# Kernel tuning notes

Measured on AMD Instinct MI355X. Metric: run time of the kernel, lower is better.

The kernel has to match this reference:

```python
import jax, jax.numpy as jnp
import numpy as np

DIM = 512
HEADS = 8
DIM_HEAD = 64
HIDDEN = HEADS * DIM_HEAD  # 512
SCALE = DIM_HEAD ** -0.5
EPS = 1e-5


def setup_inputs() -> dict:
    key = jax.random.key(0)
    ks = jax.random.split(key, 6)
    B, N = 4, 8192
    x = jax.random.normal(ks[0], (B, DIM, N), dtype=jnp.float32)
    ln_w = jnp.ones((DIM,), dtype=jnp.float32)
    ln_b = jnp.zeros((DIM,), dtype=jnp.float32)
    # stored as (in, out) so y = x @ W
    w_qkv = jax.random.normal(ks[1], (DIM, 3 * HIDDEN), dtype=jnp.float32) * (DIM ** -0.5)
    w_out = jax.random.normal(ks[2], (HIDDEN, DIM), dtype=jnp.float32) * (HIDDEN ** -0.5)
    b_out = jnp.zeros((DIM,), dtype=jnp.float32)
    return {"x": x, "ln_w": ln_w, "ln_b": ln_b, "w_qkv": w_qkv, "w_out": w_out, "b_out": b_out}


def _forward(x, ln_w, ln_b, w_qkv, w_out, b_out):
    B, D, N = x.shape
    h = jnp.swapaxes(x, 1, 2)  # b n d
    # LayerNorm over last dim
    mu = jnp.mean(h, axis=-1, keepdims=True)
    var = jnp.var(h, axis=-1, keepdims=True)
    h = (h - mu) * jax.lax.rsqrt(var + EPS) * ln_w + ln_b
    qkv = h @ w_qkv  # b n 3*hidden
    q, k, v = jnp.split(qkv, 3, axis=-1)
    # b n (h d) -> b h n d
    reshape = lambda t: jnp.swapaxes(t.reshape(B, N, HEADS, DIM_HEAD), 1, 2)
    q, k, v = reshape(q), reshape(k), reshape(v)
    q = jax.nn.softmax(q * SCALE, axis=-2)  # softmax over tokens n
    k = jax.nn.softmax(k, axis=-1)          # softmax over features d
    context = jnp.einsum('bhnd,bhne->bhde', k, v)  # small d x e per head
    out = jnp.einsum('bhde,bhnd->bhen', context, q)
    # b h e n -> b n (h e)
    out = jnp.swapaxes(out, 1, 3).reshape(B, N, HIDDEN)  # bhen -> bneh? careful: need (h e)
    # redo correctly: bhen -> b n h e -> b n (h e)
    # (the line above gives b n e h; compute properly instead)
    return out


def reference(x, ln_w, ln_b, w_qkv, w_out, b_out):
    B, D, N = x.shape
    h = jnp.swapaxes(x, 1, 2)  # b n d
    mu = jnp.mean(h, axis=-1, keepdims=True)
    var = jnp.var(h, axis=-1, keepdims=True)
    h = (h - mu) * jax.lax.rsqrt(var + EPS) * ln_w + ln_b
    qkv = h @ w_qkv  # b n 3*hidden
    q, k, v = jnp.split(qkv, 3, axis=-1)
    reshape = lambda t: jnp.swapaxes(t.reshape(B, N, HEADS, DIM_HEAD), 1, 2)  # b h n d
    q, k, v = reshape(q), reshape(k), reshape(v)
    q = jax.nn.softmax(q * SCALE, axis=-2)  # over tokens
    k = jax.nn.softmax(k, axis=-1)          # over head-dim
    context = jnp.einsum('bhnd,bhne->bhde', k, v)
    out = jnp.einsum('bhde,bhnd->bnhe', context, q)  # b n h e
    out = out.reshape(B, N, HIDDEN)  # (h e) concatenated per head
    out = out @ w_out + b_out  # b n dim
    return jnp.swapaxes(out, 1, 2)  # b dim n
```

## Files before the change

kernel.cpp:

```cpp
#include <hip/hip_runtime.h>

#define B_   4
#define N_   8192
#define D_   512
#define NH   8
#define DH   64
#define HID  512

typedef unsigned short u16;
typedef __attribute__((ext_vector_type(8))) short  bf16x8;
typedef __attribute__((ext_vector_type(8))) unsigned short u16x8;
typedef __attribute__((ext_vector_type(4))) float  f32x4;

__device__ __forceinline__ float bf2f(u16 u) {
  unsigned int i = ((unsigned int)u) << 16;
  return __builtin_bit_cast(float, i);
}
__device__ __forceinline__ u16 f2bf(float f) {
  unsigned int i = __builtin_bit_cast(unsigned int, f);
  i += 0x7fff + ((i >> 16) & 1);
  return (u16)(i >> 16);
}

#define GLOAD16(g, l) \
  __builtin_amdgcn_global_load_lds((const __attribute__((address_space(1))) void*)(g), \
                                   (__attribute__((address_space(3))) void*)(l), 16, 0, 0)

__global__ __launch_bounds__(256) void transpose_f2b(const float* __restrict__ in,
                                                     u16* __restrict__ out,
                                                     int rows, int cols) {
  int idx = blockIdx.x * 256 + threadIdx.x;
  if (idx < rows * cols) {
    int c = idx / rows, r = idx - c * rows;
    out[idx] = f2bf(in[r * cols + c]);
  }
}

__global__ __launch_bounds__(256) void ln_kernel(const float* __restrict__ x,
                                                 const float* __restrict__ lw,
                                                 const float* __restrict__ lb,
                                                 u16* __restrict__ h) {
  __shared__ u16 xs[32 * 520];
  __shared__ float red[2][8][32];
  __shared__ float murs[2][32];
  __shared__ float lws[512], lbs[512];
  int b = blockIdx.y, n0 = blockIdx.x * 32;
  int t = threadIdx.x;
  lws[t] = lw[t]; lws[t + 256] = lw[t + 256];
  lbs[t] = lb[t]; lbs[t + 256] = lb[t + 256];
  int tok = t & 31, dp = t >> 5;
  const float* xp = x + (long)b * D_ * N_ + n0 + tok;
  float s = 0.f, s2 = 0.f;
#pragma unroll 8
  for (int i = 0; i < 64; i++) {
    int d = dp * 64 + i;
    float v = xp[(long)d * N_];
    s += v; s2 += v * v;
    xs[tok * 520 + d] = f2bf(v);
  }
  red[0][dp][tok] = s; red[1][dp][tok] = s2;
  __syncthreads();
  if (t < 32) {
    float S1 = 0.f, S2 = 0.f;
#pragma unroll
    for (int i = 0; i < 8; i++) { S1 += red[0][i][t]; S2 += red[1][i][t]; }
    float mu = S1 * (1.0f / 512.0f);
    float var = S2 * (1.0f / 512.0f) - mu * mu;
    murs[0][t] = mu; murs[1][t] = rsqrtf(var + 1e-5f);
  }
  __syncthreads();
  int row = t >> 3, seg = t & 7;
  float mu = murs[0][row], rs = murs[1][row];
  u16* hp = h + ((long)b * N_ + n0 + row) * D_ + seg * 64;
  const u16* xr = xs + row * 520 + seg * 64;
#pragma unroll
  for (int c = 0; c < 8; c++) {
    u16x8 in8 = *(const u16x8*)(xr + c * 8);
    u16x8 o;
#pragma unroll
    for (int i = 0; i < 8; i++) {
      int d = seg * 64 + c * 8 + i;
      o[i] = f2bf((bf2f(in8[i]) - mu) * rs * lws[d] + lbs[d]);
    }
    *(u16x8*)(hp + c * 8) = o;
  }
}

__global__ __launch_bounds__(256) void gemm1(const u16* __restrict__ A,
                                             const u16* __restrict__ B,
                                             u16* __restrict__ qexp,
                                             u16* __restrict__ expkT,
                                             u16* __restrict__ vT,
                                             float* __restrict__ S,
                                             float* __restrict__ Z) {
  const int K = 512;
  __shared__ u16 As[128 * 32];
  __shared__ u16 Bs[128 * 32];
  __shared__ u16 Cs[128 * 136];
  int m0 = blockIdx.y * 128, n0 = blockIdx.x * 128;
  int tid = threadIdx.x, wave = tid >> 6, lane = tid & 63;
  int l15 = lane & 15, qd = lane >> 4;

  int ra0 = tid >> 2,          qa0 = (tid & 3) ^ ((ra0 >> 1) & 3);
  int ra1 = (tid + 256) >> 2,  qa1 = (tid & 3) ^ ((ra1 >> 1) & 3);
  const u16* gA0 = A + (long)(m0 + ra0) * K + qa0 * 8;
  const u16* gA1 = A + (long)(m0 + ra1) * K + qa1 * 8;
  const u16* gB0 = B + (long)(n0 + ra0) * K + qa0 * 8;
  const u16* gB1 = B + (long)(n0 + ra1) * K + qa1 * 8;
  u16* lA0 = As + wave * 512;
  u16* lA1 = As + 2048 + wave * 512;
  u16* lB0 = Bs + wave * 512;
  u16* lB1 = Bs + 2048 + wave * 512;

  int wm = wave & 1, wn = wave >> 1;
  int aoff[4], boff[4];
#pragma unroll
  for (int i = 0; i < 4; i++) {
    int r = wm * 64 + i * 16 + l15;
    aoff[i] = r * 32 + ((qd ^ ((r >> 1) & 3)) * 8);
    int rb = wn * 64 + i * 16 + l15;
    boff[i] = rb * 32 + ((qd ^ ((rb >> 1) & 3)) * 8);
  }

  f32x4 zero = {0.f, 0.f, 0.f, 0.f};
  f32x4 acc[4][4];
#pragma unroll
  for (int i = 0; i < 4; i++)
#pragma unroll
    for (int j = 0; j < 4; j++) acc[i][j] = zero;

  for (int k0 = 0; k0 < K; k0 += 32) {
    __syncthreads();
    GLOAD16(gA0 + k0, lA0);
    GLOAD16(gA1 + k0, lA1);
    GLOAD16(gB0 + k0, lB0);
    GLOAD16(gB1 + k0, lB1);
    __syncthreads();
    bf16x8 af[4], bf[4];
#pragma unroll
    for (int i = 0; i < 4; i++) {
      af[i] = *(const bf16x8*)(As + aoff[i]);
      bf[i] = *(const bf16x8*)(Bs + boff[i]);
    }
#pragma unroll
    for (int i = 0; i < 4; i++)
#pragma unroll
      for (int j = 0; j < 4; j++)
        acc[i][j] = __builtin_amdgcn_mfma_f32_16x16x32_bf16(af[i], bf[j], acc[i][j], 0, 0, 0);
  }

  int third = n0 >> 9;
  int n0t = n0 & 511;
  int b = m0 >> 13;
  int tloc = m0 & 8191;

  if (third == 0) {
#pragma unroll
    for (int i = 0; i < 4; i++)
#pragma unroll
      for (int j = 0; j < 4; j++)
#pragma unroll
        for (int r = 0; r < 4; r++) acc[i][j][r] = __expf(acc[i][j][r] * 0.125f);
#pragma unroll
    for (int j = 0; j < 4; j++) {
      float ps = 0.f;
#pragma unroll
      for (int i = 0; i < 4; i++)
#pragma unroll
        for (int r = 0; r < 4; r++) ps += acc[i][j][r];
      ps += __shfl_xor(ps, 16);
      ps += __shfl_xor(ps, 32);
      if (qd == 0) atomicAdd(S + b * 512 + n0t + wn * 64 + j * 16 + l15, ps);
    }
  } else if (third == 1) {
#pragma unroll
    for (int i = 0; i < 4; i++)
#pragma unroll
      for (int j = 0; j < 4; j++)
#pragma unroll
        for (int r = 0; r < 4; r++) acc[i][j][r] = __expf(acc[i][j][r]);
    int head = (n0t >> 6) + wn;
#pragma unroll
    for (int i = 0; i < 4; i++)
#pragma unroll
      for (int r = 0; r < 4; r++) {
        float rs = acc[i][0][r] + acc[i][1][r] + acc[i][2][r] + acc[i][3][r];
        rs += __shfl_xor(rs, 1);
        rs += __shfl_xor(rs, 2);
        rs += __shfl_xor(rs, 4);
        rs += __shfl_xor(rs, 8);
        if (l15 == 0)
          atomicAdd(Z + ((long)b * NH + head) * 8192 + tloc + wm * 64 + i * 16 + qd * 4 + r, rs);
      }
  }

  if (third == 0) {
#pragma unroll
    for (int i = 0; i < 4; i++)
#pragma unroll
      for (int r = 0; r < 4; r++)
#pragma unroll
        for (int j = 0; j < 4; j++)
          Cs[(wm * 64 + i * 16 + qd * 4 + r) * 136 + wn * 64 + j * 16 + l15] =
              f2bf(acc[i][j][r]);
  } else {
#pragma unroll
    for (int i = 0; i < 4; i++)
#pragma unroll
      for (int r = 0; r < 4; r++)
#pragma unroll
        for (int j = 0; j < 4; j++)
          Cs[(wn * 64 + j * 16 + l15) * 136 + wm * 64 + i * 16 + qd * 4 + r] =
              f2bf(acc[i][j][r]);
  }
  __syncthreads();

  u16* dst; long ldg;
  if (third == 0)      { dst = qexp  + ((long)b * N_ + tloc) * 512 + n0t;  ldg = 512; }
  else if (third == 1) { dst = expkT + ((long)b * 512 + n0t) * 8192 + tloc; ldg = 8192; }
  else                 { dst = vT    + ((long)b * 512 + n0t) * 8192 + tloc; ldg = 8192; }

#pragma unroll
  for (int outer = 0; outer < 2; outer++) {
    int row = outer * 64 + wave * 16 + (lane >> 2);
    int seg = lane & 3;
    const u16* src = Cs + row * 136;
    u16* dp = dst + (long)row * ldg;
#pragma unroll
    for (int p = 0; p < 4; p++)
      *(uint4*)(dp + p * 32 + seg * 8) = *(const uint4*)(src + p * 32 + seg * 8);
  }
}

__global__ __launch_bounds__(256) void zrecip(float* __restrict__ Z) {
  int i = blockIdx.x * 256 + threadIdx.x;
  Z[i] = 1.0f / Z[i];
}

__global__ __launch_bounds__(256) void ctx_kernel(const u16* __restrict__ expkT,
                                                  const u16* __restrict__ vT,
                                                  const float* __restrict__ Zr,
                                                  float* __restrict__ ctx) {
  __shared__ u16 As[64 * 128];
  __shared__ u16 Bs[64 * 128];
  int kc = blockIdx.x, hh = blockIdx.y, b = blockIdx.z;
  int t = threadIdx.x, w = t >> 6, l = t & 63, l15 = l & 15, qd = l >> 4;
  long nbase = (long)kc * 512;
  const u16* Abase = expkT + ((long)b * 512 + hh * 64) * 8192 + nbase;
  const u16* Bbase = vT   + ((long)b * 512 + hh * 64) * 8192 + nbase;
  const float* Zb = Zr + ((long)b * NH + hh) * 8192 + nbase;

  f32x4 zero = {0.f, 0.f, 0.f, 0.f};
  f32x4 acc[4] = {zero, zero, zero, zero};

  int brow = t >> 2;
  for (int s = 0; s < 4; s++) {
    long ko = (long)s * 128;
    __syncthreads();
#pragma unroll
    for (int si = 0; si < 4; si++) {
      int qq = si * 4 + w;
      int row = qq * 4 + (l >> 4);
      int gs = (l & 15) ^ (row & 15);
      GLOAD16(Abase + (long)row * 8192 + ko + gs * 8, As + qq * 512);
    }
    {
      const u16* src = Bbase + (long)brow * 8192 + ko;
#pragma unroll
      for (int cc = 0; cc < 4; cc++) {
        int c = (t & 3) * 4 + cc;
        u16x8 v8 = *(const u16x8*)(src + c * 8);
        float4 z0 = *(const float4*)(Zb + ko + c * 8);
        float4 z1 = *(const float4*)(Zb + ko + c * 8 + 4);
        u16x8 o;
        o[0] = f2bf(bf2f(v8[0]) * z0.x); o[1] = f2bf(bf2f(v8[1]) * z0.y);
        o[2] = f2bf(bf2f(v8[2]) * z0.z); o[3] = f2bf(bf2f(v8[3]) * z0.w);
        o[4] = f2bf(bf2f(v8[4]) * z1.x); o[5] = f2bf(bf2f(v8[5]) * z1.y);
        o[6] = f2bf(bf2f(v8[6]) * z1.z); o[7] = f2bf(bf2f(v8[7]) * z1.w);
        *(u16x8*)(Bs + brow * 128 + ((c ^ (brow & 15)) * 8)) = o;
      }
    }
    __syncthreads();
#pragma unroll
    for (int kk = 0; kk < 4; kk++) {
      int ar = w * 16 + l15;
      bf16x8 af = *(const bf16x8*)(As + ar * 128 + (((kk * 4 + qd) ^ (ar & 15)) * 8));
#pragma unroll
      for (int j = 0; j < 4; j++) {
        int br = j * 16 + l15;
        bf16x8 bf8 = *(const bf16x8*)(Bs + br * 128 + (((kk * 4 + qd) ^ (br & 15)) * 8));
        acc[j] = __builtin_amdgcn_mfma_f32_16x16x32_bf16(af, bf8, acc[j], 0, 0, 0);
      }
    }
  }
  float* cp = ctx + ((long)(b * NH + hh)) * DH * DH;
#pragma unroll
  for (int j = 0; j < 4; j++)
#pragma unroll
    for (int r = 0; r < 4; r++)
      atomicAdd(cp + (w * 16 + qd * 4 + r) * 64 + j * 16 + l15, acc[j][r]);
}

__global__ __launch_bounds__(256) void mprime(const float* __restrict__ ctx,
                                              const float* __restrict__ wout,
                                              const float* __restrict__ S,
                                              u16* __restrict__ Mt) {
  __shared__ float ws[64 * 65];
  __shared__ float cs[64 * 65];
  int dt = blockIdx.x, hh = blockIdx.y, b = blockIdx.z;
  int t = threadIdx.x;
  {
    int e = t >> 2;
#pragma unroll
    for (int ii = 0; ii < 4; ii++) {
      int col = (t & 3) * 16 + ii * 4;
      float4 v = *(const float4*)(wout + (long)(hh * 64 + e) * 512 + dt * 64 + col);
      ws[e * 65 + col] = v.x; ws[e * 65 + col + 1] = v.y;
      ws[e * 65 + col + 2] = v.z; ws[e * 65 + col + 3] = v.w;
      float4 c = *(const float4*)(ctx + ((long)(b * NH + hh)) * 4096 + (long)e * 64 + col);
      cs[e * 65 + col] = c.x; cs[e * 65 + col + 1] = c.y;
      cs[e * 65 + col + 2] = c.z; cs[e * 65 + col + 3] = c.w;
    }
  }
  __syncthreads();
  int dol = t & 63, dg = t >> 6;
#pragma unroll
  for (int dd = 0; dd < 16; dd++) {
    int d = dg * 16 + dd;
    float v = 0.f;
#pragma unroll 8
    for (int e = 0; e < 64; e++) v += cs[d * 65 + e] * ws[e * 65 + dol];
    float sv = S[b * 512 + hh * 64 + d];
    Mt[(long)b * 262144 + (long)(dt * 64 + dol) * 512 + hh * 64 + d] = f2bf(v / sv);
  }
}

__global__ __launch_bounds__(256) void gemm_tn_f(const u16* __restrict__ A,
                                                 const u16* __restrict__ B,
                                                 float* __restrict__ C,
                                                 const float* __restrict__ bias,
                                                 int K, int ldc,
                                                 long sA, long sB, long sC) {
  __shared__ u16 As[128 * 32];
  __shared__ u16 Bs[128 * 32];
  long bz = blockIdx.z;
  A += bz * sA; B += bz * sB; C += bz * sC;
  int m0 = blockIdx.y * 128, n0 = blockIdx.x * 128;
  int tid = threadIdx.x, wave = tid >> 6, lane = tid & 63;
  int l15 = lane & 15, qd = lane >> 4;

  int ra0 = tid >> 2,          qa0 = (tid & 3) ^ ((ra0 >> 1) & 3);
  int ra1 = (tid + 256) >> 2,  qa1 = (tid & 3) ^ ((ra1 >> 1) & 3);
  const u16* gA0 = A + (long)(m0 + ra0) * K + qa0 * 8;
  const u16* gA1 = A + (long)(m0 + ra1) * K + qa1 * 8;
  const u16* gB0 = B + (long)(n0 + ra0) * K + qa0 * 8;
  const u16* gB1 = B + (long)(n0 + ra1) * K + qa1 * 8;
  u16* lA0 = As + wave * 512;
  u16* lA1 = As + 2048 + wave * 512;
  u16* lB0 = Bs + wave * 512;
  u16* lB1 = Bs + 2048 + wave * 512;

  int wm = wave & 1, wn = wave >> 1;
  int aoff[4], boff[4];
#pragma unroll
  for (int i = 0; i < 4; i++) {
    int r = wm * 64 + i * 16 + l15;
    aoff[i] = r * 32 + ((qd ^ ((r >> 1) & 3)) * 8);
    int rb = wn * 64 + i * 16 + l15;
    boff[i] = rb * 32 + ((qd ^ ((rb >> 1) & 3)) * 8);
  }

  f32x4 zero = {0.f, 0.f, 0.f, 0.f};
  f32x4 acc[4][4];
#pragma unroll
  for (int i = 0; i < 4; i++)
#pragma unroll
    for (int j = 0; j < 4; j++) acc[i][j] = zero;

  for (int k0 = 0; k0 < K; k0 += 32) {
    __syncthreads();
    GLOAD16(gA0 + k0, lA0);
    GLOAD16(gA1 + k0, lA1);
    GLOAD16(gB0 + k0, lB0);
    GLOAD16(gB1 + k0, lB1);
    __syncthreads();
    bf16x8 af[4], bf[4];
#pragma unroll
    for (int i = 0; i < 4; i++) {
      af[i] = *(const bf16x8*)(As + aoff[i]);
      bf[i] = *(const bf16x8*)(Bs + boff[i]);
    }
#pragma unroll
    for (int i = 0; i < 4; i++)
#pragma unroll
      for (int j = 0; j < 4; j++)
        acc[i][j] = __builtin_amdgcn_mfma_f32_16x16x32_bf16(af[i], bf[j], acc[i][j], 0, 0, 0);
  }
#pragma unroll
  for (int i = 0; i < 4; i++) {
#pragma unroll
    for (int r = 0; r < 4; r++) {
      int row = wm * 64 + i * 16 + qd * 4 + r;
      float bv = bias ? bias[m0 + row] : 0.0f;
#pragma unroll
      for (int j = 0; j < 4; j++) {
        int col = wn * 64 + j * 16 + l15;
        C[(long)(m0 + row) * ldc + n0 + col] = acc[i][j][r] + bv;
      }
    }
  }
}

extern "C" void kernel_launch(void* const* d_in, const int* in_sizes, int n_in,
                              void* d_out, int out_size, void* d_ws, size_t ws_size,
                              hipStream_t stream) {
  const float* x    = (const float*)d_in[0];
  const float* lnw  = (const float*)d_in[1];
  const float* lnb  = (const float*)d_in[2];
  const float* wqkv = (const float*)d_in[3];
  const float* wout = (const float*)d_in[4];
  const float* bout = (const float*)d_in[5];
  float* out = (float*)d_out;
  char* ws = (char*)d_ws;

  u16*  h     = (u16*)(ws + 0L);
  u16*  qexp  = (u16*)(ws + 33554432L);
  u16*  expkT = (u16*)(ws + 67108864L);
  u16*  vT    = (u16*)(ws + 100663296L);
  u16*  wqkvT = (u16*)(ws + 134217728L);
  u16*  Mt    = (u16*)(ws + 134217728L);
  float* S    = (float*)(ws + 136314880L);
  float* ctx  = (float*)(ws + 0L);
  float* Z    = (float*)d_out;

  hipMemsetAsync(S, 0, 4 * 512 * 4, stream);
  hipMemsetAsync(Z, 0, (long)B_ * NH * 8192 * 4, stream);

  transpose_f2b<<<dim3((512 * 1536 + 255) / 256), 256, 0, stream>>>(wqkv, wqkvT, 512, 1536);

  ln_kernel<<<dim3(256, 4), 256, 0, stream>>>(x, lnw, lnb, h);

  gemm1<<<dim3(12, 256), 256, 0, stream>>>(h, wqkvT, qexp, expkT, vT, S, Z);

  zrecip<<<dim3(1024), 256, 0, stream>>>(Z);

  hipMemsetAsync(ctx, 0, 4 * 8 * 64 * 64 * 4, stream);

  ctx_kernel<<<dim3(16, 8, 4), 256, 0, stream>>>(expkT, vT, Z, ctx);

  mprime<<<dim3(8, 8, 4), 256, 0, stream>>>(ctx, wout, S, Mt);

  gemm_tn_f<<<dim3(64, 4, 4), 256, 0, stream>>>(Mt, qexp, out, bout, 512, 8192,
                                                262144L, (long)8192 * 512, (long)512 * 8192);
}
```

Before: 318.4 us.

## Coalesce global stores across transpose, layernorm, gemm1 and output GEMM epilogues

```diff
diff --git a/kernel.cpp b/kernel.cpp
--- a/kernel.cpp
+++ b/kernel.cpp
@@ -29,10 +29,21 @@
 __global__ __launch_bounds__(256) void transpose_f2b(const float* __restrict__ in,
                                                      u16* __restrict__ out,
                                                      int rows, int cols) {
-  int idx = blockIdx.x * 256 + threadIdx.x;
-  if (idx < rows * cols) {
-    int c = idx / rows, r = idx - c * rows;
-    out[idx] = f2bf(in[r * cols + c]);
+  __shared__ u16 tile[64][65];
+  int c0 = blockIdx.x * 64, r0 = blockIdx.y * 64;
+  int t = threadIdx.x;
+  int rl = t >> 6, cl = t & 63;
+#pragma unroll
+  for (int i = 0; i < 16; i++) {
+    int r = i * 4 + rl;
+    tile[r][cl] = f2bf(in[(long)(r0 + r) * cols + c0 + cl]);
+  }
+  __syncthreads();
+  int c4 = t >> 6, rr = t & 63;
+#pragma unroll
+  for (int i = 0; i < 16; i++) {
+    int c = i * 4 + c4;
+    out[(long)(c0 + c) * rows + r0 + rr] = tile[rr][c];
   }
 }
 
@@ -71,18 +82,19 @@
   __syncthreads();
   int row = t >> 3, seg = t & 7;
   float mu = murs[0][row], rs = murs[1][row];
-  u16* hp = h + ((long)b * N_ + n0 + row) * D_ + seg * 64;
-  const u16* xr = xs + row * 520 + seg * 64;
+  u16* hp = h + ((long)b * N_ + n0 + row) * D_;
+  const u16* xr = xs + row * 520;
 #pragma unroll
   for (int c = 0; c < 8; c++) {
-    u16x8 in8 = *(const u16x8*)(xr + c * 8);
+    int d0 = c * 64 + seg * 8;
+    u16x8 in8 = *(const u16x8*)(xr + d0);
     u16x8 o;
 #pragma unroll
     for (int i = 0; i < 8; i++) {
-      int d = seg * 64 + c * 8 + i;
+      int d = d0 + i;
       o[i] = f2bf((bf2f(in8[i]) - mu) * rs * lws[d] + lbs[d]);
     }
-    *(u16x8*)(hp + c * 8) = o;
+    *(u16x8*)(hp + d0) = o;
   }
 }
 
@@ -220,16 +232,18 @@
   else if (third == 1) { dst = expkT + ((long)b * 512 + n0t) * 8192 + tloc; ldg = 8192; }
   else                 { dst = vT    + ((long)b * 512 + n0t) * 8192 + tloc; ldg = 8192; }
 
-#pragma unroll
-  for (int outer = 0; outer < 2; outer++) {
-    int row = outer * 64 + wave * 16 + (lane >> 2);
-    int seg = lane & 3;
-    const u16* src = Cs + row * 136;
-    u16* dp = dst + (long)row * ldg;
-#pragma unroll
-    for (int p = 0; p < 4; p++)
-      *(uint4*)(dp + p * 32 + seg * 8) = *(const uint4*)(src + p * 32 + seg * 8);
-  }
+  int seg = lane & 7;
+#pragma unroll
+  for (int outer = 0; outer < 2; outer++)
+#pragma unroll
+    for (int rr = 0; rr < 2; rr++) {
+      int row = outer * 64 + wave * 16 + rr * 8 + (lane >> 3);
+      const u16* src = Cs + row * 136;
+      u16* dp = dst + (long)row * ldg;
+#pragma unroll
+      for (int p = 0; p < 2; p++)
+        *(uint4*)(dp + p * 64 + seg * 8) = *(const uint4*)(src + p * 64 + seg * 8);
+    }
 }
 
 __global__ __launch_bounds__(256) void zrecip(float* __restrict__ Z) {
@@ -343,9 +357,10 @@
                                                  long sA, long sB, long sC) {
   __shared__ u16 As[128 * 32];
   __shared__ u16 Bs[128 * 32];
+  __shared__ float Cf[64 * 133];
   long bz = blockIdx.z;
   A += bz * sA; B += bz * sB; C += bz * sC;
-  int m0 = blockIdx.y * 128, n0 = blockIdx.x * 128;
+  int m0 = blockIdx.x * 128, n0 = blockIdx.y * 128;
   int tid = threadIdx.x, wave = tid >> 6, lane = tid & 63;
   int l15 = lane & 15, qd = lane >> 4;
 
@@ -396,17 +411,32 @@
       for (int j = 0; j < 4; j++)
         acc[i][j] = __builtin_amdgcn_mfma_f32_16x16x32_bf16(af[i], bf[j], acc[i][j], 0, 0, 0);
   }
-#pragma unroll
-  for (int i = 0; i < 4; i++) {
-#pragma unroll
-    for (int r = 0; r < 4; r++) {
-      int row = wm * 64 + i * 16 + qd * 4 + r;
-      float bv = bias ? bias[m0 + row] : 0.0f;
-#pragma unroll
-      for (int j = 0; j < 4; j++) {
-        int col = wn * 64 + j * 16 + l15;
-        C[(long)(m0 + row) * ldc + n0 + col] = acc[i][j][r] + bv;
-      }
+
+#pragma unroll
+  for (int half = 0; half < 2; half++) {
+    __syncthreads();
+    if (wm == half) {
+#pragma unroll
+      for (int i = 0; i < 4; i++)
+#pragma unroll
+        for (int r = 0; r < 4; r++) {
+          int rl = i * 16 + qd * 4 + r;
+          float bv = bias[m0 + half * 64 + rl];
+#pragma unroll
+          for (int j = 0; j < 4; j++)
+            Cf[rl * 133 + wn * 64 + j * 16 + l15] = acc[i][j][r] + bv;
+        }
+    }
+    __syncthreads();
+#pragma unroll
+    for (int z = 0; z < 2; z++) {
+      int rl = z * 32 + (tid >> 3);
+      int seg = tid & 7;
+      float* dp = C + (long)(m0 + half * 64 + rl) * ldc + n0;
+      const float* src = Cf + rl * 133;
+#pragma unroll
+      for (int p = 0; p < 4; p++)
+        *(float4*)(dp + p * 32 + seg * 4) = *(const float4*)(src + p * 32 + seg * 4);
     }
   }
 }
@@ -436,7 +466,7 @@
   hipMemsetAsync(S, 0, 4 * 512 * 4, stream);
   hipMemsetAsync(Z, 0, (long)B_ * NH * 8192 * 4, stream);
 
-  transpose_f2b<<<dim3((512 * 1536 + 255) / 256), 256, 0, stream>>>(wqkv, wqkvT, 512, 1536);
+  transpose_f2b<<<dim3(24, 8), 256, 0, stream>>>(wqkv, wqkvT, 512, 1536);
 
   ln_kernel<<<dim3(256, 4), 256, 0, stream>>>(x, lnw, lnb, h);
 
@@ -450,6 +480,6 @@
 
   mprime<<<dim3(8, 8, 4), 256, 0, stream>>>(ctx, wout, S, Mt);
 
-  gemm_tn_f<<<dim3(64, 4, 4), 256, 0, stream>>>(Mt, qexp, out, bout, 512, 8192,
+  gemm_tn_f<<<dim3(4, 64, 4), 256, 0, stream>>>(Mt, qexp, out, bout, 512, 8192,
                                                 262144L, (long)8192 * 512, (long)512 * 8192);
 }
```

Result: no change. 312.7 us (-1.8%).
